# Kernel optimization log

Measured on AMD Instinct MI355X. Metric: run time of the kernel, lower is better.

## Reference

```python
import jax, jax.numpy as jnp
import numpy as np

EPS = 1e-6

def gram_schmidt_orthonormalize(U, eps=EPS):
    # U: [B, K, D] -> orthonormalized along K, vectorized over batch
    B, K, D = U.shape
    vs = []
    for i in range(K):
        v = U[:, i]  # [B, D]
        for vj in vs:
            coeff = jnp.sum(v * vj, axis=1, keepdims=True) / (jnp.sum(vj * vj, axis=1, keepdims=True) + eps)
            v = v - coeff * vj
        norm = jnp.maximum(jnp.linalg.norm(v, axis=1, keepdims=True), eps)
        vs.append(v / norm)
    return jnp.stack(vs, axis=1)  # [B, K, D]

def setup_inputs() -> dict:
    key = jax.random.key(0)
    ks = jax.random.split(key, 14)
    B, IN, H1, H2, OUT, E, G = 4096, 1024, 2048, 2048, 512, 8, 256
    s = 0.02
    return {
        "x":   jax.random.normal(ks[0], (B, IN), jnp.float32),
        "W1":  jax.random.normal(ks[1], (E, IN, H1), jnp.float32) * s,
        "b1":  jnp.zeros((E, H1), jnp.float32),
        "W2":  jax.random.normal(ks[2], (E, H1, H2), jnp.float32) * s,
        "b2":  jnp.zeros((E, H2), jnp.float32),
        "W3":  jax.random.normal(ks[3], (E, H2, OUT), jnp.float32) * s,
        "b3":  jnp.zeros((E, OUT), jnp.float32),
        "Wg1": jax.random.normal(ks[4], (IN, G), jnp.float32) * s,
        "bg1": jnp.zeros((G,), jnp.float32),
        "Wg2": jax.random.normal(ks[5], (G, E), jnp.float32) * s,
        "bg2": jnp.zeros((E,), jnp.float32),
        "Wo":  jax.random.normal(ks[6], (OUT, 1), jnp.float32) * s,
        "bo":  jnp.zeros((1,), jnp.float32),
    }

def reference(x, W1, b1, W2, b2, W3, b3, Wg1, bg1, Wg2, bg2, Wo, bo):
    # Expert MLPs, batched over expert axis e: [B,E,h]
    h = jax.nn.relu(jnp.einsum('bi,eih->beh', x, W1) + b1)
    h = jax.nn.relu(jnp.einsum('beh,ehk->bek', h, W2) + b2)
    expert_outputs = jnp.einsum('bek,ekd->bed', h, W3) + b3  # [B, E, D]
    # Gating network: MLP + softmax over experts
    g = jax.nn.relu(x @ Wg1 + bg1)
    gate_weights = jax.nn.softmax(g @ Wg2 + bg2, axis=-1)  # [B, E]
    # Per-sample Gram-Schmidt across experts, weighted combine
    ortho = gram_schmidt_orthonormalize(expert_outputs)  # [B, E, D]
    combined = jnp.einsum('bed,be->bd', ortho, gate_weights)  # [B, D]
    final = combined @ Wo + bo  # [B, 1]
    return (final, 0.0)
```

## Files before the change

kernel.cpp:

```cpp
#include <hip/hip_runtime.h>
#include <hip/hip_bf16.h>

#define DEVINL __device__ __forceinline__

constexpr int Bsz = 4096, INF = 1024, H1 = 2048, H2 = 2048, OUTD = 512, NE = 8, G = 256;

typedef __attribute__((ext_vector_type(8))) short bf16x8;
typedef __attribute__((ext_vector_type(4))) float f32x4;

DEVINL unsigned short f2bf(float f) {
  unsigned int u = __float_as_uint(f);
  u = (u + 0x7FFFu + ((u >> 16) & 1u)) >> 16;
  return (unsigned short)u;
}
DEVINL float bf2f(unsigned short h) { return __uint_as_float((unsigned int)h << 16); }

DEVINL void gload16(const void* g, void* l) {
  __builtin_amdgcn_global_load_lds(
      (const __attribute__((address_space(1))) void*)g,
      (__attribute__((address_space(3))) void*)l, 16, 0, 0);
}

DEVINL float waveAllSum(float v) {
#pragma unroll
  for (int m = 32; m > 0; m >>= 1) v += __shfl_xor(v, m, 64);
  return v;
}

__global__ __launch_bounds__(256) void pack_act(const float* __restrict__ in,
                                                unsigned short* __restrict__ hi,
                                                unsigned short* __restrict__ lo) {
  size_t i = ((size_t)blockIdx.x * 256 + threadIdx.x) * 4;
  float4 v = *(const float4*)&in[i];
  short4 h, l;
  h.x = f2bf(v.x); l.x = f2bf(v.x - bf2f(h.x));
  h.y = f2bf(v.y); l.y = f2bf(v.y - bf2f(h.y));
  h.z = f2bf(v.z); l.z = f2bf(v.z - bf2f(h.z));
  h.w = f2bf(v.w); l.w = f2bf(v.w - bf2f(h.w));
  *(short4*)&hi[i] = h;
  *(short4*)&lo[i] = l;
}

__global__ __launch_bounds__(256) void pack_wt(const float* __restrict__ W,
                                               unsigned short* __restrict__ Th,
                                               unsigned short* __restrict__ Tl,
                                               int K, int N) {
  __shared__ float t[32][33];
  const int e = blockIdx.z;
  W += (size_t)e * K * N;
  Th += (size_t)e * N * K;
  Tl += (size_t)e * N * K;
  const int n0 = blockIdx.x * 32, k0 = blockIdx.y * 32;
  const int r = threadIdx.x >> 3, c = (threadIdx.x & 7) * 4;
  float4 v = *(const float4*)&W[(size_t)(k0 + r) * N + n0 + c];
  t[r][c + 0] = v.x; t[r][c + 1] = v.y; t[r][c + 2] = v.z; t[r][c + 3] = v.w;
  __syncthreads();
  float o0 = t[c + 0][r], o1 = t[c + 1][r], o2 = t[c + 2][r], o3 = t[c + 3][r];
  short4 h, l;
  h.x = f2bf(o0); l.x = f2bf(o0 - bf2f(h.x));
  h.y = f2bf(o1); l.y = f2bf(o1 - bf2f(h.y));
  h.z = f2bf(o2); l.z = f2bf(o2 - bf2f(h.z));
  h.w = f2bf(o3); l.w = f2bf(o3 - bf2f(h.w));
  *(short4*)&Th[(size_t)(n0 + r) * K + k0 + c] = h;
  *(short4*)&Tl[(size_t)(n0 + r) * K + k0 + c] = l;
}

#define PHASE_MID()                                    \
  __builtin_amdgcn_sched_barrier(0);                   \
  __builtin_amdgcn_s_barrier();                        \
  asm volatile("s_waitcnt lgkmcnt(0)" ::: "memory");   \
  __builtin_amdgcn_sched_barrier(0)
#define PHASE_END()                                    \
  __builtin_amdgcn_sched_barrier(0);                   \
  __builtin_amdgcn_s_barrier()
#define QUAD(IH, JH, BH, BL)                                                   \
  __builtin_amdgcn_s_setprio(1);                                               \
  _Pragma("unroll") for (int i = 0; i < 4; ++i) {                              \
    _Pragma("unroll") for (int j = 0; j < 2; ++j) {                            \
      f32x4 a = acc[(IH)*4 + i][(JH)*2 + j];                                   \
      a = __builtin_amdgcn_mfma_f32_16x16x32_bf16(BH[j], ah[i], a, 0, 0, 0);   \
      a = __builtin_amdgcn_mfma_f32_16x16x32_bf16(BL[j], ah[i], a, 0, 0, 0);   \
      a = __builtin_amdgcn_mfma_f32_16x16x32_bf16(BH[j], al[i], a, 0, 0, 0);   \
      acc[(IH)*4 + i][(JH)*2 + j] = a;                                         \
    }                                                                          \
  }                                                                            \
  __builtin_amdgcn_s_setprio(0);

template <int RELU, int OUTF32>
__global__ __launch_bounds__(512, 2) void gemm_bf16x3_8ph(
    const unsigned short* __restrict__ Ahi, const unsigned short* __restrict__ Alo,
    const unsigned short* __restrict__ Bhi, const unsigned short* __restrict__ Blo,
    const float* __restrict__ bias,
    unsigned short* __restrict__ Chi, unsigned short* __restrict__ Clo,
    float* __restrict__ Cf, int M, int N, int K, size_t strideAe) {
  const int e = blockIdx.x;
  Ahi += (size_t)e * strideAe;
  Alo += (size_t)e * strideAe;
  Bhi += (size_t)e * (size_t)N * K;
  Blo += (size_t)e * (size_t)N * K;
  bias += (size_t)e * N;
  if (OUTF32) Cf += (size_t)e * (size_t)M * N;
  else { Chi += (size_t)e * (size_t)M * N; Clo += (size_t)e * (size_t)M * N; }

  const int bm = blockIdx.y * 256, bn = blockIdx.z * 256;
  __shared__ __align__(16) char ldsb[131072];
  const int lane = threadIdx.x & 63, wid = threadIdx.x >> 6;
  const int wm = wid >> 2, wn = wid & 3;
  const int l15 = lane & 15, l4 = lane >> 4;
  const int bhalf = wn >> 1, jn = wn & 1;

  f32x4 acc[8][4];
#pragma unroll
  for (int i = 0; i < 8; ++i)
#pragma unroll
    for (int j = 0; j < 4; ++j) acc[i][j] = (f32x4){0.f, 0.f, 0.f, 0.f};

  const int nt = K / 32;

  auto stageA = [&](const unsigned short* src, int T, int ldsOp) {
    const int s = T & 1;
#pragma unroll
    for (int q = 0; q < 2; ++q) {
      const int g = wid * 2 + q;
      gload16(src + (size_t)(bm + g * 16 + l15) * K + T * 32 + l4 * 8,
              ldsb + ldsOp + s * 16384 + g * 1024);
    }
  };
  auto stageB = [&](int T, int h) {
    const int s = T & 1;
#pragma unroll
    for (int q = 0; q < 2; ++q) {
      const int g = wid * 2 + q;
      const unsigned short* src = (g < 8) ? Bhi : Blo;
      const int f = g & 7;
      gload16(src + (size_t)(bn + h * 128 + f * 16 + l15) * K + T * 32 + l4 * 8,
              ldsb + ((g < 8) ? 65536 : 98304) + s * 16384 + h * 8192 + f * 1024);
    }
  };

  bf16x8 ah[4], al[4], b0h[2], b0l[2], b1h[2], b1l[2];
  auto readA = [&](int s, int ih) {
#pragma unroll
    for (int i = 0; i < 4; ++i) {
      const int off = s * 16384 + wm * 8192 + (ih * 4 + i) * 1024 + lane * 16;
      ah[i] = *(const bf16x8*)(ldsb + off);
      al[i] = *(const bf16x8*)(ldsb + 32768 + off);
    }
  };
  auto readB = [&](int s, int jh, bf16x8* bh, bf16x8* bl) {
#pragma unroll
    for (int j = 0; j < 2; ++j) {
      const int off = s * 16384 + bhalf * 8192 + (jn * 4 + jh * 2 + j) * 1024 + lane * 16;
      bh[j] = *(const bf16x8*)(ldsb + 65536 + off);
      bl[j] = *(const bf16x8*)(ldsb + 98304 + off);
    }
  };

  stageB(0, 0); stageB(0, 1);
  stageA(Ahi, 0, 0); stageA(Alo, 0, 32768);
  stageB(1, 0); stageB(1, 1);
  asm volatile("s_waitcnt vmcnt(4)" ::: "memory");
  __builtin_amdgcn_sched_barrier(0);
  __builtin_amdgcn_s_barrier();

  for (int t = 0; t < nt; ++t) {
    const int s = t & 1;
    readA(s, 0);
    readB(s, 0, b0h, b0l);
    if (t + 1 < nt) stageA(Ahi, t + 1, 0);
    PHASE_MID();
    QUAD(0, 0, b0h, b0l);
    PHASE_END();
    readB(s, 1, b1h, b1l);
    if (t + 1 < nt) stageA(Alo, t + 1, 32768);
    PHASE_MID();
    QUAD(0, 1, b1h, b1l);
    PHASE_END();
    readA(s, 1);
    if (t + 2 < nt) stageB(t + 2, 0);
    PHASE_MID();
    QUAD(1, 0, b0h, b0l);
    PHASE_END();
    if (t + 2 < nt) stageB(t + 2, 1);
    PHASE_MID();
    QUAD(1, 1, b1h, b1l);
    asm volatile("s_waitcnt vmcnt(4)" ::: "memory");
    __builtin_amdgcn_sched_barrier(0);
    PHASE_END();
  }

#pragma unroll
  for (int i = 0; i < 8; ++i) {
    const int grow = bm + wm * 128 + i * 16 + l15;
#pragma unroll
    for (int j = 0; j < 4; ++j) {
      const int gcol = bn + wn * 64 + j * 16 + l4 * 4;
      const float4 bb = *(const float4*)&bias[gcol];
      float v0 = acc[i][j][0] + bb.x, v1 = acc[i][j][1] + bb.y;
      float v2 = acc[i][j][2] + bb.z, v3 = acc[i][j][3] + bb.w;
      if (RELU) {
        v0 = fmaxf(v0, 0.f); v1 = fmaxf(v1, 0.f);
        v2 = fmaxf(v2, 0.f); v3 = fmaxf(v3, 0.f);
      }
      if (OUTF32) {
        *(float4*)&Cf[(size_t)grow * N + gcol] = make_float4(v0, v1, v2, v3);
      } else {
        short4 h, l;
        h.x = f2bf(v0); l.x = f2bf(v0 - bf2f(h.x));
        h.y = f2bf(v1); l.y = f2bf(v1 - bf2f(h.y));
        h.z = f2bf(v2); l.z = f2bf(v2 - bf2f(h.z));
        h.w = f2bf(v3); l.w = f2bf(v3 - bf2f(h.w));
        *(short4*)&Chi[(size_t)grow * N + gcol] = h;
        *(short4*)&Clo[(size_t)grow * N + gcol] = l;
      }
    }
  }
}

__global__ __launch_bounds__(256) void gate1_kernel(
    const float* __restrict__ x, const float* __restrict__ Wg1,
    const float* __restrict__ bg1, float* __restrict__ g) {
  __shared__ float xs[8 * 1024];
  const int b0 = blockIdx.x * 8;
  const float* xp = x + (size_t)b0 * INF;
  for (int idx = threadIdx.x * 4; idx < 8 * 1024; idx += 1024)
    *(float4*)&xs[idx] = *(const float4*)&xp[idx];
  __syncthreads();
  const int t = threadIdx.x;
  float acc[8] = {0, 0, 0, 0, 0, 0, 0, 0};
  for (int i = 0; i < INF; ++i) {
    float w = Wg1[(size_t)i * G + t];
#pragma unroll
    for (int r = 0; r < 8; ++r) acc[r] = fmaf(xs[r * 1024 + i], w, acc[r]);
  }
  const float bb = bg1[t];
#pragma unroll
  for (int r = 0; r < 8; ++r)
    g[(size_t)(b0 + r) * G + t] = fmaxf(acc[r] + bb, 0.0f);
}

__global__ __launch_bounds__(64) void gate2_kernel(
    const float* __restrict__ g, const float* __restrict__ Wg2,
    const float* __restrict__ bg2, float* __restrict__ gw) {
  const int b = blockIdx.x, lane = threadIdx.x;
  float4 gv = *(const float4*)(g + (size_t)b * G + lane * 4);
  float p[8];
#pragma unroll
  for (int e = 0; e < 8; ++e) {
    int j = lane * 4;
    float s = gv.x * Wg2[(j + 0) * 8 + e] + gv.y * Wg2[(j + 1) * 8 + e] +
              gv.z * Wg2[(j + 2) * 8 + e] + gv.w * Wg2[(j + 3) * 8 + e];
    p[e] = waveAllSum(s);
  }
  if (lane == 0) {
    float l[8];
    float mx = -1e30f;
#pragma unroll
    for (int e = 0; e < 8; ++e) {
      l[e] = p[e] + bg2[e];
      mx = fmaxf(mx, l[e]);
    }
    float sum = 0.0f;
#pragma unroll
    for (int e = 0; e < 8; ++e) {
      l[e] = expf(l[e] - mx);
      sum += l[e];
    }
    float inv = 1.0f / sum;
#pragma unroll
    for (int e = 0; e < 8; ++e) gw[(size_t)b * 8 + e] = l[e] * inv;
  }
}

__global__ __launch_bounds__(256) void gs_kernel(
    const float* __restrict__ eo, const float* __restrict__ gw,
    const float* __restrict__ Wo, const float* __restrict__ bo,
    float* __restrict__ out, int CB) {
  const int lane = threadIdx.x & 63;
  const int b = blockIdx.x * 4 + (threadIdx.x >> 6);
  const size_t ES = (size_t)CB * OUTD;
  const float* base = eo + (size_t)b * OUTD + lane * 8;
  float vs[8][8];
  float denom[8];
#pragma unroll
  for (int i = 0; i < 8; ++i) {
    float cur[8];
    float4 u0 = *(const float4*)(base + (size_t)i * ES);
    float4 u1 = *(const float4*)(base + (size_t)i * ES + 4);
    cur[0] = u0.x; cur[1] = u0.y; cur[2] = u0.z; cur[3] = u0.w;
    cur[4] = u1.x; cur[5] = u1.y; cur[6] = u1.z; cur[7] = u1.w;
#pragma unroll
    for (int j = 0; j < i; ++j) {
      float dp = 0.0f;
#pragma unroll
      for (int d = 0; d < 8; ++d) dp = fmaf(cur[d], vs[j][d], dp);
      dp = waveAllSum(dp);
      float coeff = dp / (denom[j] + 1e-6f);
#pragma unroll
      for (int d = 0; d < 8; ++d) cur[d] = fmaf(-coeff, vs[j][d], cur[d]);
    }
    float nn = 0.0f;
#pragma unroll
    for (int d = 0; d < 8; ++d) nn = fmaf(cur[d], cur[d], nn);
    nn = waveAllSum(nn);
    float inv = 1.0f / fmaxf(sqrtf(nn), 1e-6f);
#pragma unroll
    for (int d = 0; d < 8; ++d) vs[i][d] = cur[d] * inv;
    float dd = 0.0f;
#pragma unroll
    for (int d = 0; d < 8; ++d) dd = fmaf(vs[i][d], vs[i][d], dd);
    denom[i] = waveAllSum(dd);
  }
  float gwv[8];
#pragma unroll
  for (int e = 0; e < 8; ++e) gwv[e] = gw[(size_t)b * 8 + e];
  float part = 0.0f;
#pragma unroll
  for (int d = 0; d < 8; ++d) {
    float c = 0.0f;
#pragma unroll
    for (int e = 0; e < 8; ++e) c = fmaf(vs[e][d], gwv[e], c);
    part = fmaf(c, Wo[lane * 8 + d], part);
  }
  part = waveAllSum(part);
  if (lane == 0) out[b] = part + bo[0];
}

extern "C" void kernel_launch(void* const* d_in, const int* in_sizes, int n_in,
                              void* d_out, int out_size, void* d_ws, size_t ws_size,
                              hipStream_t stream) {
  const float* x   = (const float*)d_in[0];
  const float* W1  = (const float*)d_in[1];
  const float* b1  = (const float*)d_in[2];
  const float* W2  = (const float*)d_in[3];
  const float* b2  = (const float*)d_in[4];
  const float* W3  = (const float*)d_in[5];
  const float* b3  = (const float*)d_in[6];
  const float* Wg1 = (const float*)d_in[7];
  const float* bg1 = (const float*)d_in[8];
  const float* Wg2 = (const float*)d_in[9];
  const float* bg2 = (const float*)d_in[10];
  const float* Wo  = (const float*)d_in[11];
  const float* bo  = (const float*)d_in[12];
  float* out = (float*)d_out;

  typedef unsigned short u16;
  char* p = (char*)d_ws;
  float* gw = (float*)p;          p += (size_t)(128u << 10);
  float* g  = (float*)p;          p += (size_t)(4u << 20);
  u16* xhi = (u16*)p;             p += (size_t)Bsz * INF * 2;
  u16* xlo = (u16*)p;             p += (size_t)Bsz * INF * 2;
  u16* w1h = (u16*)p;             p += (size_t)NE * H1 * INF * 2;
  u16* w1l = (u16*)p;             p += (size_t)NE * H1 * INF * 2;
  u16* w2h = (u16*)p;             p += (size_t)NE * H2 * H1 * 2;
  u16* w2l = (u16*)p;             p += (size_t)NE * H2 * H1 * 2;
  u16* w3h = (u16*)p;             p += (size_t)NE * OUTD * H2 * 2;
  u16* w3l = (u16*)p;             p += (size_t)NE * OUTD * H2 * 2;
  const size_t fixedBytes = (size_t)(p - (char*)d_ws);

  int CB = 4096;
  while (CB > 256 && fixedBytes + (size_t)CB * (size_t)(128u << 10) > ws_size) CB >>= 1;
  u16* h1h = (u16*)p;
  u16* h1l = h1h + (size_t)NE * CB * H1;
  u16* h2h = h1l + (size_t)NE * CB * H1;
  u16* h2l = h2h + (size_t)NE * CB * H2;
  float* eo = (float*)h1h;

  hipMemsetAsync(d_out, 0, (size_t)out_size * sizeof(float), stream);

  pack_act<<<(Bsz * INF) / 1024, 256, 0, stream>>>(x, xhi, xlo);
  pack_wt<<<dim3(H1 / 32, INF / 32, NE), 256, 0, stream>>>(W1, w1h, w1l, INF, H1);
  pack_wt<<<dim3(H2 / 32, H1 / 32, NE), 256, 0, stream>>>(W2, w2h, w2l, H1, H2);
  pack_wt<<<dim3(OUTD / 32, H2 / 32, NE), 256, 0, stream>>>(W3, w3h, w3l, H2, OUTD);

  gate1_kernel<<<Bsz / 8, 256, 0, stream>>>(x, Wg1, bg1, g);
  gate2_kernel<<<Bsz, 64, 0, stream>>>(g, Wg2, bg2, gw);

  for (int c0 = 0; c0 < Bsz; c0 += CB) {
    gemm_bf16x3_8ph<1, 0><<<dim3(NE, CB / 256, H1 / 256), 512, 0, stream>>>(
        xhi + (size_t)c0 * INF, xlo + (size_t)c0 * INF, w1h, w1l, b1,
        h1h, h1l, nullptr, CB, H1, INF, (size_t)0);
    gemm_bf16x3_8ph<1, 0><<<dim3(NE, CB / 256, H2 / 256), 512, 0, stream>>>(
        h1h, h1l, w2h, w2l, b2, h2h, h2l, nullptr, CB, H2, H1, (size_t)CB * H1);
    gemm_bf16x3_8ph<0, 1><<<dim3(NE, CB / 256, OUTD / 256), 512, 0, stream>>>(
        h2h, h2l, w3h, w3l, b3, nullptr, nullptr, eo, CB, OUTD, H2, (size_t)CB * H2);
    gs_kernel<<<CB / 4, 256, 0, stream>>>(eo, gw + (size_t)c0 * NE, Wo, bo,
                                          out + c0, CB);
  }
}
```

Measured before the change: 1.617 ms.

## Switch GEMMs to 32x32x16 MFMA and add 128-row tile kernel for W3 layer

Replaces the 16x16x32 bf16 MFMA tiles with 32x32x16 MFMA instructions in the split-bf16 (hi/lo, three-product) expert GEMMs, reorganizing LDS staging and fragment reads for 32-row tiles. This lowers instruction count and LDS fragment reads per FLOP. A separate kernel for the final layer (N=512) uses 128-row M tiles with a three-slot B buffer, doubling the block count so the small output GEMM fills the device better. The risk is changed register pressure and LDS access patterns that may cause bank conflicts.

```diff
diff --git a/kernel.cpp b/kernel.cpp
--- a/kernel.cpp
+++ b/kernel.cpp
@@ -6,14 +6,16 @@
 constexpr int Bsz = 4096, INF = 1024, H1 = 2048, H2 = 2048, OUTD = 512, NE = 8, G = 256;
 
 typedef __attribute__((ext_vector_type(8))) short bf16x8;
-typedef __attribute__((ext_vector_type(4))) float f32x4;
-
-DEVINL unsigned short f2bf(float f) {
+typedef __attribute__((ext_vector_type(16))) float f32x16;
+
+typedef unsigned short u16;
+
+DEVINL u16 f2bf(float f) {
   unsigned int u = __float_as_uint(f);
   u = (u + 0x7FFFu + ((u >> 16) & 1u)) >> 16;
-  return (unsigned short)u;
-}
-DEVINL float bf2f(unsigned short h) { return __uint_as_float((unsigned int)h << 16); }
+  return (u16)u;
+}
+DEVINL float bf2f(u16 h) { return __uint_as_float((unsigned int)h << 16); }
 
 DEVINL void gload16(const void* g, void* l) {
   __builtin_amdgcn_global_load_lds(
@@ -27,9 +29,25 @@
   return v;
 }
 
+DEVINL f32x16 mfma3(bf16x8 bh, bf16x8 bl, bf16x8 ah, bf16x8 al, f32x16 c) {
+  c = __builtin_amdgcn_mfma_f32_32x32x16_bf16(bh, ah, c, 0, 0, 0);
+  c = __builtin_amdgcn_mfma_f32_32x32x16_bf16(bl, ah, c, 0, 0, 0);
+  c = __builtin_amdgcn_mfma_f32_32x32x16_bf16(bh, al, c, 0, 0, 0);
+  return c;
+}
+
+#define PHASE_MID()                                    \
+  __builtin_amdgcn_sched_barrier(0);                   \
+  __builtin_amdgcn_s_barrier();                        \
+  asm volatile("s_waitcnt lgkmcnt(0)" ::: "memory");   \
+  __builtin_amdgcn_sched_barrier(0)
+#define PHASE_END()                                    \
+  __builtin_amdgcn_sched_barrier(0);                   \
+  __builtin_amdgcn_s_barrier()
+
 __global__ __launch_bounds__(256) void pack_act(const float* __restrict__ in,
-                                                unsigned short* __restrict__ hi,
-                                                unsigned short* __restrict__ lo) {
+                                                u16* __restrict__ hi,
+                                                u16* __restrict__ lo) {
   size_t i = ((size_t)blockIdx.x * 256 + threadIdx.x) * 4;
   float4 v = *(const float4*)&in[i];
   short4 h, l;
@@ -42,8 +60,8 @@
 }
 
 __global__ __launch_bounds__(256) void pack_wt(const float* __restrict__ W,
-                                               unsigned short* __restrict__ Th,
-                                               unsigned short* __restrict__ Tl,
+                                               u16* __restrict__ Th,
+                                               u16* __restrict__ Tl,
                                                int K, int N) {
   __shared__ float t[32][33];
   const int e = blockIdx.z;
@@ -65,64 +83,43 @@
   *(short4*)&Tl[(size_t)(n0 + r) * K + k0 + c] = l;
 }
 
-#define PHASE_MID()                                    \
-  __builtin_amdgcn_sched_barrier(0);                   \
-  __builtin_amdgcn_s_barrier();                        \
-  asm volatile("s_waitcnt lgkmcnt(0)" ::: "memory");   \
-  __builtin_amdgcn_sched_barrier(0)
-#define PHASE_END()                                    \
-  __builtin_amdgcn_sched_barrier(0);                   \
-  __builtin_amdgcn_s_barrier()
-#define QUAD(IH, JH, BH, BL)                                                   \
-  __builtin_amdgcn_s_setprio(1);                                               \
-  _Pragma("unroll") for (int i = 0; i < 4; ++i) {                              \
-    _Pragma("unroll") for (int j = 0; j < 2; ++j) {                            \
-      f32x4 a = acc[(IH)*4 + i][(JH)*2 + j];                                   \
-      a = __builtin_amdgcn_mfma_f32_16x16x32_bf16(BH[j], ah[i], a, 0, 0, 0);   \
-      a = __builtin_amdgcn_mfma_f32_16x16x32_bf16(BL[j], ah[i], a, 0, 0, 0);   \
-      a = __builtin_amdgcn_mfma_f32_16x16x32_bf16(BH[j], al[i], a, 0, 0, 0);   \
-      acc[(IH)*4 + i][(JH)*2 + j] = a;                                         \
-    }                                                                          \
-  }                                                                            \
-  __builtin_amdgcn_s_setprio(0);
-
-template <int RELU, int OUTF32>
-__global__ __launch_bounds__(512, 2) void gemm_bf16x3_8ph(
-    const unsigned short* __restrict__ Ahi, const unsigned short* __restrict__ Alo,
-    const unsigned short* __restrict__ Bhi, const unsigned short* __restrict__ Blo,
+__global__ __launch_bounds__(512, 2) void gemm32_256(
+    const u16* __restrict__ Ahi, const u16* __restrict__ Alo,
+    const u16* __restrict__ Bhi, const u16* __restrict__ Blo,
     const float* __restrict__ bias,
-    unsigned short* __restrict__ Chi, unsigned short* __restrict__ Clo,
-    float* __restrict__ Cf, int M, int N, int K, size_t strideAe) {
+    u16* __restrict__ Chi, u16* __restrict__ Clo,
+    int M, int N, int K, size_t strideAe) {
   const int e = blockIdx.x;
   Ahi += (size_t)e * strideAe;
   Alo += (size_t)e * strideAe;
   Bhi += (size_t)e * (size_t)N * K;
   Blo += (size_t)e * (size_t)N * K;
   bias += (size_t)e * N;
-  if (OUTF32) Cf += (size_t)e * (size_t)M * N;
-  else { Chi += (size_t)e * (size_t)M * N; Clo += (size_t)e * (size_t)M * N; }
+  Chi += (size_t)e * (size_t)M * N;
+  Clo += (size_t)e * (size_t)M * N;
 
   const int bm = blockIdx.y * 256, bn = blockIdx.z * 256;
   __shared__ __align__(16) char ldsb[131072];
   const int lane = threadIdx.x & 63, wid = threadIdx.x >> 6;
   const int wm = wid >> 2, wn = wid & 3;
-  const int l15 = lane & 15, l4 = lane >> 4;
-  const int bhalf = wn >> 1, jn = wn & 1;
-
-  f32x4 acc[8][4];
-#pragma unroll
-  for (int i = 0; i < 8; ++i)
-#pragma unroll
-    for (int j = 0; j < 4; ++j) acc[i][j] = (f32x4){0.f, 0.f, 0.f, 0.f};
+  const int l31 = lane & 31, lk = lane >> 5;
+
+  f32x16 acc[4][2];
+#pragma unroll
+  for (int i = 0; i < 4; ++i)
+#pragma unroll
+    for (int j = 0; j < 2; ++j)
+#pragma unroll
+      for (int q = 0; q < 16; ++q) acc[i][j][q] = 0.f;
 
   const int nt = K / 32;
 
-  auto stageA = [&](const unsigned short* src, int T, int ldsOp) {
+  auto stageA = [&](const u16* src, int T, int ldsOp) {
     const int s = T & 1;
 #pragma unroll
     for (int q = 0; q < 2; ++q) {
       const int g = wid * 2 + q;
-      gload16(src + (size_t)(bm + g * 16 + l15) * K + T * 32 + l4 * 8,
+      gload16(src + (size_t)(bm + (g >> 1) * 32 + l31) * K + T * 32 + (g & 1) * 16 + lk * 8,
               ldsb + ldsOp + s * 16384 + g * 1024);
     }
   };
@@ -131,30 +128,42 @@
 #pragma unroll
     for (int q = 0; q < 2; ++q) {
       const int g = wid * 2 + q;
-      const unsigned short* src = (g < 8) ? Bhi : Blo;
+      const u16* src = (g < 8) ? Bhi : Blo;
       const int f = g & 7;
-      gload16(src + (size_t)(bn + h * 128 + f * 16 + l15) * K + T * 32 + l4 * 8,
+      gload16(src + (size_t)(bn + h * 128 + (f >> 1) * 32 + l31) * K + T * 32 + (f & 1) * 16 + lk * 8,
               ldsb + ((g < 8) ? 65536 : 98304) + s * 16384 + h * 8192 + f * 1024);
     }
   };
 
-  bf16x8 ah[4], al[4], b0h[2], b0l[2], b1h[2], b1l[2];
+  bf16x8 ah[2][2], al[2][2], b0h[2], b0l[2], b1h[2], b1l[2];
   auto readA = [&](int s, int ih) {
 #pragma unroll
-    for (int i = 0; i < 4; ++i) {
-      const int off = s * 16384 + wm * 8192 + (ih * 4 + i) * 1024 + lane * 16;
-      ah[i] = *(const bf16x8*)(ldsb + off);
-      al[i] = *(const bf16x8*)(ldsb + 32768 + off);
-    }
+    for (int i = 0; i < 2; ++i)
+#pragma unroll
+      for (int ks = 0; ks < 2; ++ks) {
+        const int off = s * 16384 + ((wm * 4 + ih * 2 + i) * 2 + ks) * 1024 + lane * 16;
+        ah[i][ks] = *(const bf16x8*)(ldsb + off);
+        al[i][ks] = *(const bf16x8*)(ldsb + 32768 + off);
+      }
   };
   auto readB = [&](int s, int jh, bf16x8* bh, bf16x8* bl) {
 #pragma unroll
-    for (int j = 0; j < 2; ++j) {
-      const int off = s * 16384 + bhalf * 8192 + (jn * 4 + jh * 2 + j) * 1024 + lane * 16;
-      bh[j] = *(const bf16x8*)(ldsb + 65536 + off);
-      bl[j] = *(const bf16x8*)(ldsb + 98304 + off);
-    }
-  };
+    for (int ks = 0; ks < 2; ++ks) {
+      const int off = s * 16384 + ((wn * 2 + jh) * 2 + ks) * 1024 + lane * 16;
+      bh[ks] = *(const bf16x8*)(ldsb + 65536 + off);
+      bl[ks] = *(const bf16x8*)(ldsb + 98304 + off);
+    }
+  };
+
+#define QUAD32(IH, JH, BH, BL)                                              \
+  __builtin_amdgcn_s_setprio(1);                                            \
+  _Pragma("unroll") for (int i = 0; i < 2; ++i) {                           \
+    _Pragma("unroll") for (int ks = 0; ks < 2; ++ks) {                      \
+      acc[(IH)*2 + i][JH] =                                                 \
+          mfma3(BH[ks], BL[ks], ah[i][ks], al[i][ks], acc[(IH)*2 + i][JH]); \
+    }                                                                       \
+  }                                                                         \
+  __builtin_amdgcn_s_setprio(0);
 
   stageB(0, 0); stageB(0, 1);
   stageA(Ahi, 0, 0); stageA(Alo, 0, 32768);
@@ -169,49 +178,176 @@
     readB(s, 0, b0h, b0l);
     if (t + 1 < nt) stageA(Ahi, t + 1, 0);
     PHASE_MID();
-    QUAD(0, 0, b0h, b0l);
+    QUAD32(0, 0, b0h, b0l);
     PHASE_END();
     readB(s, 1, b1h, b1l);
     if (t + 1 < nt) stageA(Alo, t + 1, 32768);
     PHASE_MID();
-    QUAD(0, 1, b1h, b1l);
+    QUAD32(0, 1, b1h, b1l);
     PHASE_END();
     readA(s, 1);
     if (t + 2 < nt) stageB(t + 2, 0);
     PHASE_MID();
-    QUAD(1, 0, b0h, b0l);
+    QUAD32(1, 0, b0h, b0l);
     PHASE_END();
     if (t + 2 < nt) stageB(t + 2, 1);
     PHASE_MID();
-    QUAD(1, 1, b1h, b1l);
+    QUAD32(1, 1, b1h, b1l);
     asm volatile("s_waitcnt vmcnt(4)" ::: "memory");
     __builtin_amdgcn_sched_barrier(0);
     PHASE_END();
   }
-
-#pragma unroll
-  for (int i = 0; i < 8; ++i) {
-    const int grow = bm + wm * 128 + i * 16 + l15;
-#pragma unroll
-    for (int j = 0; j < 4; ++j) {
-      const int gcol = bn + wn * 64 + j * 16 + l4 * 4;
-      const float4 bb = *(const float4*)&bias[gcol];
-      float v0 = acc[i][j][0] + bb.x, v1 = acc[i][j][1] + bb.y;
-      float v2 = acc[i][j][2] + bb.z, v3 = acc[i][j][3] + bb.w;
-      if (RELU) {
-        v0 = fmaxf(v0, 0.f); v1 = fmaxf(v1, 0.f);
-        v2 = fmaxf(v2, 0.f); v3 = fmaxf(v3, 0.f);
-      }
-      if (OUTF32) {
-        *(float4*)&Cf[(size_t)grow * N + gcol] = make_float4(v0, v1, v2, v3);
-      } else {
+#undef QUAD32
+
+#pragma unroll
+  for (int rt = 0; rt < 4; ++rt) {
+    const int grow = bm + wm * 128 + rt * 32 + l31;
+#pragma unroll
+    for (int ct = 0; ct < 2; ++ct) {
+      const int gcol0 = bn + wn * 64 + ct * 32;
+      const f32x16 a = acc[rt][ct];
+#pragma unroll
+      for (int q = 0; q < 4; ++q) {
+        const int c0 = gcol0 + q * 8 + lk * 4;
+        const float4 bb = *(const float4*)&bias[c0];
+        float v0 = fmaxf(a[q * 4 + 0] + bb.x, 0.f);
+        float v1 = fmaxf(a[q * 4 + 1] + bb.y, 0.f);
+        float v2 = fmaxf(a[q * 4 + 2] + bb.z, 0.f);
+        float v3 = fmaxf(a[q * 4 + 3] + bb.w, 0.f);
         short4 h, l;
         h.x = f2bf(v0); l.x = f2bf(v0 - bf2f(h.x));
         h.y = f2bf(v1); l.y = f2bf(v1 - bf2f(h.y));
         h.z = f2bf(v2); l.z = f2bf(v2 - bf2f(h.z));
         h.w = f2bf(v3); l.w = f2bf(v3 - bf2f(h.w));
-        *(short4*)&Chi[(size_t)grow * N + gcol] = h;
-        *(short4*)&Clo[(size_t)grow * N + gcol] = l;
+        *(short4*)&Chi[(size_t)grow * N + c0] = h;
+        *(short4*)&Clo[(size_t)grow * N + c0] = l;
+      }
+    }
+  }
+}
+
+__global__ __launch_bounds__(512, 2) void gemm32_128(
+    const u16* __restrict__ Ahi, const u16* __restrict__ Alo,
+    const u16* __restrict__ Bhi, const u16* __restrict__ Blo,
+    const float* __restrict__ bias, float* __restrict__ Cf,
+    int M, int N, int K, size_t strideAe) {
+  const int e = blockIdx.x;
+  Ahi += (size_t)e * strideAe;
+  Alo += (size_t)e * strideAe;
+  Bhi += (size_t)e * (size_t)N * K;
+  Blo += (size_t)e * (size_t)N * K;
+  bias += (size_t)e * N;
+  Cf += (size_t)e * (size_t)M * N;
+
+  const int bm = blockIdx.y * 128, bn = blockIdx.z * 256;
+  __shared__ __align__(16) char ldsb[131072];
+  const int lane = threadIdx.x & 63, wid = threadIdx.x >> 6;
+  const int wm = wid >> 2, wn = wid & 3;
+  const int l31 = lane & 31, lk = lane >> 5;
+
+  f32x16 acc[2][2];
+#pragma unroll
+  for (int i = 0; i < 2; ++i)
+#pragma unroll
+    for (int j = 0; j < 2; ++j)
+#pragma unroll
+      for (int q = 0; q < 16; ++q) acc[i][j][q] = 0.f;
+
+  const int nt = K / 32;
+
+  auto stageA2 = [&](int T) {
+    const int s = T & 1;
+#pragma unroll
+    for (int q = 0; q < 2; ++q) {
+      const int g = wid * 2 + q;
+      const u16* src = (g < 8) ? Ahi : Alo;
+      const int f = g & 7;
+      gload16(src + (size_t)(bm + (f >> 1) * 32 + l31) * K + T * 32 + (f & 1) * 16 + lk * 8,
+              ldsb + ((g < 8) ? 0 : 16384) + s * 8192 + f * 1024);
+    }
+  };
+  auto stageB2 = [&](int T, int slot) {
+#pragma unroll
+    for (int q = 0; q < 4; ++q) {
+      const int g = wid * 4 + q;
+      const u16* src = (g < 16) ? Bhi : Blo;
+      const int f = g & 15;
+      gload16(src + (size_t)(bn + (f >> 1) * 32 + l31) * K + T * 32 + (f & 1) * 16 + lk * 8,
+              ldsb + ((g < 16) ? 32768 : 81920) + slot * 16384 + f * 1024);
+    }
+  };
+
+  bf16x8 ah[2][2], al[2][2], b0h[2], b0l[2], b1h[2], b1l[2];
+  auto readA2 = [&](int s) {
+#pragma unroll
+    for (int i = 0; i < 2; ++i)
+#pragma unroll
+      for (int ks = 0; ks < 2; ++ks) {
+        const int off = s * 8192 + ((wm * 2 + i) * 2 + ks) * 1024 + lane * 16;
+        ah[i][ks] = *(const bf16x8*)(ldsb + off);
+        al[i][ks] = *(const bf16x8*)(ldsb + 16384 + off);
+      }
+  };
+  auto readB2 = [&](int bs, int jh, bf16x8* bh, bf16x8* bl) {
+#pragma unroll
+    for (int ks = 0; ks < 2; ++ks) {
+      const int off = bs * 16384 + ((wn * 2 + jh) * 2 + ks) * 1024 + lane * 16;
+      bh[ks] = *(const bf16x8*)(ldsb + 32768 + off);
+      bl[ks] = *(const bf16x8*)(ldsb + 81920 + off);
+    }
+  };
+
+#define QUAD2(JH, BH, BL)                                          \
+  __builtin_amdgcn_s_setprio(1);                                   \
+  _Pragma("unroll") for (int i = 0; i < 2; ++i) {                  \
+    _Pragma("unroll") for (int ks = 0; ks < 2; ++ks) {             \
+      acc[i][JH] = mfma3(BH[ks], BL[ks], ah[i][ks], al[i][ks], acc[i][JH]); \
+    }                                                              \
+  }                                                                \
+  __builtin_amdgcn_s_setprio(0);
+
+  stageA2(0);
+  stageB2(0, 0);
+  stageB2(1, 1);
+  asm volatile("s_waitcnt vmcnt(4)" ::: "memory");
+  __builtin_amdgcn_sched_barrier(0);
+  __builtin_amdgcn_s_barrier();
+
+  int bs = 0;
+  for (int t = 0; t < nt; ++t) {
+    const int sa = t & 1;
+    int bs2 = bs - 1; if (bs2 < 0) bs2 = 2;
+    readA2(sa);
+    readB2(bs, 0, b0h, b0l);
+    if (t + 1 < nt) stageA2(t + 1);
+    if (t + 2 < nt) stageB2(t + 2, bs2);
+    PHASE_MID();
+    QUAD2(0, b0h, b0l);
+    PHASE_END();
+    readB2(bs, 1, b1h, b1l);
+    PHASE_MID();
+    QUAD2(1, b1h, b1l);
+    asm volatile("s_waitcnt vmcnt(4)" ::: "memory");
+    __builtin_amdgcn_sched_barrier(0);
+    PHASE_END();
+    bs = (bs == 2) ? 0 : bs + 1;
+  }
+#undef QUAD2
+
+#pragma unroll
+  for (int rt = 0; rt < 2; ++rt) {
+    const int grow = bm + wm * 64 + rt * 32 + l31;
+#pragma unroll
+    for (int ct = 0; ct < 2; ++ct) {
+      const int gcol0 = bn + wn * 64 + ct * 32;
+      const f32x16 a = acc[rt][ct];
+#pragma unroll
+      for (int q = 0; q < 4; ++q) {
+        const int c0 = gcol0 + q * 8 + lk * 4;
+        const float4 bb = *(const float4*)&bias[c0];
+        *(float4*)&Cf[(size_t)grow * N + c0] =
+            make_float4(a[q * 4 + 0] + bb.x, a[q * 4 + 1] + bb.y,
+                        a[q * 4 + 2] + bb.z, a[q * 4 + 3] + bb.w);
       }
     }
   }
@@ -344,7 +480,6 @@
   const float* bo  = (const float*)d_in[12];
   float* out = (float*)d_out;
 
-  typedef unsigned short u16;
   char* p = (char*)d_ws;
   float* gw = (float*)p;          p += (size_t)(128u << 10);
   float* g  = (float*)p;          p += (size_t)(4u << 20);
@@ -377,13 +512,13 @@
   gate2_kernel<<<Bsz, 64, 0, stream>>>(g, Wg2, bg2, gw);
 
   for (int c0 = 0; c0 < Bsz; c0 += CB) {
-    gemm_bf16x3_8ph<1, 0><<<dim3(NE, CB / 256, H1 / 256), 512, 0, stream>>>(
+    gemm32_256<<<dim3(NE, CB / 256, H1 / 256), 512, 0, stream>>>(
         xhi + (size_t)c0 * INF, xlo + (size_t)c0 * INF, w1h, w1l, b1,
-        h1h, h1l, nullptr, CB, H1, INF, (size_t)0);
-    gemm_bf16x3_8ph<1, 0><<<dim3(NE, CB / 256, H2 / 256), 512, 0, stream>>>(
-        h1h, h1l, w2h, w2l, b2, h2h, h2l, nullptr, CB, H2, H1, (size_t)CB * H1);
-    gemm_bf16x3_8ph<0, 1><<<dim3(NE, CB / 256, OUTD / 256), 512, 0, stream>>>(
-        h2h, h2l, w3h, w3l, b3, nullptr, nullptr, eo, CB, OUTD, H2, (size_t)CB * H2);
+        h1h, h1l, CB, H1, INF, (size_t)0);
+    gemm32_256<<<dim3(NE, CB / 256, H2 / 256), 512, 0, stream>>>(
+        h1h, h1l, w2h, w2l, b2, h2h, h2l, CB, H2, H1, (size_t)CB * H1);
+    gemm32_128<<<dim3(NE, CB / 128, OUTD / 256), 512, 0, stream>>>(
+        h2h, h2l, w3h, w3l, b3, eo, CB, OUTD, H2, (size_t)CB * H2);
     gs_kernel<<<CB / 4, 256, 0, stream>>>(eo, gw + (size_t)c0 * NE, Wo, bo,
                                           out + c0, CB);
   }
```

After: 1.888 ms. 16.8% more time.
